# Performance work log

Hardware: AMD Instinct MI355X
Metric: run time of the kernel (lower is better)

The kernel has to match this reference:

```python
import jax, jax.numpy as jnp
import numpy as np

# Config: AydinConfig(hidden_dim=1024, intermediate_dim=2048, num_experts=8, top_k=2)
E, H, I, K = 8, 1024, 2048, 2
B, S = 4, 2048


def setup_inputs() -> dict:
    key = jax.random.key(0)
    k1, k2, k3, k4 = jax.random.split(key, 4)
    x = jax.random.normal(k1, (B, S, H), dtype=jnp.float32)
    # nn.Linear(H, E, bias=False): weight shape (E, H), default init ~ U(-1/sqrt(H), 1/sqrt(H))
    router_w = jax.random.uniform(k2, (E, H), dtype=jnp.float32,
                                  minval=-1.0, maxval=1.0) / np.sqrt(H).astype(np.float32)
    # normal init, std=0.02 (reset_parameters)
    w13 = jax.random.normal(k3, (E, H, 2 * I), dtype=jnp.float32) * 0.02
    w2 = jax.random.normal(k4, (E, I, H), dtype=jnp.float32) * 0.02
    return {"x": x, "router_w": router_w, "w13": w13, "w2": w2}


def reference(x, router_w, w13, w2):
    # Router: logits (B,S,E) -> softmax -> top-k with renormalized weights
    logits = jnp.einsum('bsh,eh->bse', x, router_w)
    probs = jax.nn.softmax(logits, axis=-1)
    weights, indices = jax.lax.top_k(probs, K)            # (B,S,K)
    weights = weights / (weights.sum(axis=-1, keepdims=True) + 1e-6)
    # Expert SwiGLU, computed densely over all experts then gathered.
    # Same math as the torch per-token weight gather, but avoids the
    # (B,S,K,H,2I) gathered-weight blowup.
    h13 = jnp.einsum('bsh,ehi->bsei', x, w13)             # (B,S,E,2I)
    gate, up = jnp.split(h13, 2, axis=-1)                 # (B,S,E,I) each
    h = jax.nn.silu(gate) * up
    y = jnp.einsum('bsei,eih->bseh', h, w2)               # (B,S,E,H)
    # Gather top-k expert outputs and combine with routing weights
    y_sel = jnp.take_along_axis(y, indices[..., None], axis=2)  # (B,S,K,H)
    return (y_sel * weights[..., None]).sum(axis=2)       # (B,S,H)
```

## Files before the change

kernel.cpp:

```cpp
#include <hip/hip_runtime.h>
#include <hip/hip_bf16.h>
#include <math.h>

#define NEXP 8
#define HD 1024
#define ID 2048
#define NTOK 8192
#define NROWS 16384

typedef __bf16 bf16_t;
typedef __bf16 bf16x8 __attribute__((ext_vector_type(8)));
typedef float f32x4 __attribute__((ext_vector_type(4)));

#define BK 64
#define MAXT1 72
#define MAXT2 136

__device__ __forceinline__ void gl16(const void* g, void* l) {
    __builtin_amdgcn_global_load_lds(
        (const __attribute__((address_space(1))) unsigned int*)g,
        (__attribute__((address_space(3))) unsigned int*)l, 16, 0, 0);
}

__global__ __launch_bounds__(256)
void router_kernel(const float* __restrict__ x, const float* __restrict__ rw,
                   bf16_t* __restrict__ xb, int* __restrict__ topk_idx,
                   float* __restrict__ topk_w)
{
    const int t = blockIdx.x;
    const int tid = threadIdx.x;
    const float4 xv = ((const float4*)(x + (size_t)t * HD))[tid];
    float acc[NEXP];
#pragma unroll
    for (int e = 0; e < NEXP; ++e) {
        const float4 w4 = ((const float4*)(rw + e * HD))[tid];
        acc[e] = xv.x * w4.x + xv.y * w4.y + xv.z * w4.z + xv.w * w4.w;
    }
    bf16_t tmp[4] = {(bf16_t)xv.x, (bf16_t)xv.y, (bf16_t)xv.z, (bf16_t)xv.w};
    *(uint2*)(xb + (size_t)t * HD + tid * 4) = *(const uint2*)tmp;

    __shared__ float red[4][NEXP];
    const int lane = tid & 63, wv = tid >> 6;
#pragma unroll
    for (int e = 0; e < NEXP; ++e) {
        float v = acc[e];
#pragma unroll
        for (int off = 32; off >= 1; off >>= 1) v += __shfl_down(v, off, 64);
        if (lane == 0) red[wv][e] = v;
    }
    __syncthreads();
    if (tid == 0) {
        float lg[NEXP], mx = -1e30f;
#pragma unroll
        for (int e = 0; e < NEXP; ++e) {
            lg[e] = red[0][e] + red[1][e] + red[2][e] + red[3][e];
            mx = fmaxf(mx, lg[e]);
        }
        float p[NEXP], s = 0.f;
#pragma unroll
        for (int e = 0; e < NEXP; ++e) { p[e] = __expf(lg[e] - mx); s += p[e]; }
        const float inv = 1.f / s;
#pragma unroll
        for (int e = 0; e < NEXP; ++e) p[e] *= inv;
        int i0 = 0; float p0 = p[0];
#pragma unroll
        for (int e = 1; e < NEXP; ++e) if (p[e] > p0) { p0 = p[e]; i0 = e; }
        int i1 = -1; float p1 = -1.f;
#pragma unroll
        for (int e = 0; e < NEXP; ++e) if (e != i0 && p[e] > p1) { p1 = p[e]; i1 = e; }
        const float d = 1.f / (p0 + p1 + 1e-6f);
        topk_idx[t * 2 + 0] = i0; topk_idx[t * 2 + 1] = i1;
        topk_w[t * 2 + 0] = p0 * d; topk_w[t * 2 + 1] = p1 * d;
    }
}

__global__ __launch_bounds__(256)
void count_kernel(const int* __restrict__ topk_idx, int* __restrict__ counts)
{
    __shared__ int lc[NEXP];
    const int tid = threadIdx.x;
    if (tid < NEXP) lc[tid] = 0;
    __syncthreads();
    const int t = blockIdx.x * 256 + tid;
    atomicAdd(&lc[topk_idx[t * 2 + 0]], 1);
    atomicAdd(&lc[topk_idx[t * 2 + 1]], 1);
    __syncthreads();
    if (tid < NEXP) atomicAdd(&counts[tid], lc[tid]);
}

__global__ void scan_kernel(const int* __restrict__ counts, int* __restrict__ offsets,
                            int* __restrict__ cursor,
                            unsigned* __restrict__ map256, unsigned* __restrict__ map128)
{
    __shared__ int tb2[NEXP + 1], tb1[NEXP + 1];
    if (threadIdx.x == 0) {
        int s = 0, t2 = 0, t1 = 0;
        for (int e = 0; e < NEXP; ++e) {
            offsets[e] = s; cursor[e] = s; s += counts[e];
            tb2[e] = t2; t2 += (counts[e] + 255) >> 8;
            tb1[e] = t1; t1 += (counts[e] + 127) >> 7;
        }
        tb2[NEXP] = t2; tb1[NEXP] = t1;
    }
    __syncthreads();
    for (int i = threadIdx.x; i < MAXT1; i += 64) {
        unsigned v = 0xFFFFFFFFu;
#pragma unroll
        for (int e = 0; e < NEXP; ++e)
            if (i >= tb2[e] && i < tb2[e + 1]) v = ((unsigned)e << 16) | (unsigned)(i - tb2[e]);
        map256[i] = v;
    }
    for (int i = threadIdx.x; i < MAXT2; i += 64) {
        unsigned v = 0xFFFFFFFFu;
#pragma unroll
        for (int e = 0; e < NEXP; ++e)
            if (i >= tb1[e] && i < tb1[e + 1]) v = ((unsigned)e << 16) | (unsigned)(i - tb1[e]);
        map128[i] = v;
    }
}

__global__ __launch_bounds__(256)
void scatter_kernel(const int* __restrict__ topk_idx, const float* __restrict__ topk_w,
                    int* __restrict__ cursor, int* __restrict__ token_list,
                    float* __restrict__ row_w, int* __restrict__ row_pos)
{
    __shared__ int lc[NEXP], gbase[NEXP];
    const int tid = threadIdx.x;
    if (tid < NEXP) lc[tid] = 0;
    __syncthreads();
    const int t = blockIdx.x * 256 + tid;
    const int e0 = topk_idx[t * 2 + 0], e1 = topk_idx[t * 2 + 1];
    const int lp0 = atomicAdd(&lc[e0], 1);
    const int lp1 = atomicAdd(&lc[e1], 1);
    __syncthreads();
    if (tid < NEXP) gbase[tid] = atomicAdd(&cursor[tid], lc[tid]);
    __syncthreads();
    const int p0 = gbase[e0] + lp0, p1 = gbase[e1] + lp1;
    token_list[p0] = t; row_w[p0] = topk_w[t * 2 + 0]; row_pos[t * 2 + 0] = p0;
    token_list[p1] = t; row_w[p1] = topk_w[t * 2 + 1]; row_pos[t * 2 + 1] = p1;
}

__global__ __launch_bounds__(256)
void precast_kernel(const float* __restrict__ src, bf16_t* __restrict__ dst,
                    int K, int N)
{
    const int e = blockIdx.z;
    src += (size_t)e * K * N;
    dst += (size_t)e * K * N;
    const int n0 = blockIdx.x * 64, k0 = blockIdx.y * 64;
    __shared__ float tile[64][65];
    const int tid = threadIdx.x;
    const int tx = (tid & 15) * 4, ty = tid >> 4;
#pragma unroll
    for (int p = 0; p < 4; ++p) {
        const float4 v = *(const float4*)(src + (size_t)(k0 + ty + p * 16) * N + n0 + tx);
        tile[ty + p * 16][tx + 0] = v.x;
        tile[ty + p * 16][tx + 1] = v.y;
        tile[ty + p * 16][tx + 2] = v.z;
        tile[ty + p * 16][tx + 3] = v.w;
    }
    __syncthreads();
    const int n = tid >> 2, kc = (tid & 3) * 16;
    bf16_t outv[16];
#pragma unroll
    for (int j = 0; j < 16; ++j) outv[j] = (bf16_t)tile[kc + j][n];
    bf16_t* d = dst + (size_t)(n0 + n) * K + k0 + kc;
    *(uint4*)d = *(uint4*)outv;
    *(uint4*)(d + 8) = *((uint4*)outv + 1);
}

__global__ __launch_bounds__(512)
void gemm1_kernel(const bf16_t* __restrict__ xb, const bf16_t* __restrict__ w13b,
                  const int* __restrict__ offsets, const int* __restrict__ counts,
                  const int* __restrict__ token_list,
                  const unsigned* __restrict__ tile_map, bf16_t* __restrict__ hbuf)
{
    const unsigned tm = tile_map[blockIdx.y];
    if (tm == 0xFFFFFFFFu) return;
    const int e = (int)(tm >> 16), mt = (int)(tm & 0xFFFFu);
    const int rows = counts[e];
    const int row_base = offsets[e];
    const int r0 = mt * 256;
    const int n0 = blockIdx.x * 64;

    __shared__ alignas(16) bf16_t As[256][64];
    __shared__ alignas(16) bf16_t Bg[64][64];
    __shared__ alignas(16) bf16_t Bu[64][64];

    const int tid = threadIdx.x;
    const int lane = tid & 63;
    const int wv = tid >> 6;
    const int wr = wv >> 1, wc = wv & 1;
    const int ln15 = lane & 15, q = lane >> 4;
    const int x7 = ln15 & 7;
    const int c0 = ((q ^ x7)) * 8;
    const int c1 = c0 ^ 32;

    const int srow = tid >> 3;
    const int scol = ((tid & 7) ^ ((tid >> 3) & 7)) * 8;
    const bf16_t* ap[4];
#pragma unroll
    for (int p = 0; p < 4; ++p) {
        int gr = row_base + r0 + p * 64 + srow;
        if (gr > NROWS - 1) gr = NROWS - 1;
        ap[p] = xb + (size_t)token_list[gr] * HD + scol;
    }
    const bf16_t* wb = w13b + (size_t)e * HD * (2 * ID);
    const bf16_t* bgp = wb + (size_t)(n0 + srow) * HD + scol;
    const bf16_t* bup = wb + (size_t)(ID + n0 + srow) * HD + scol;
    bf16_t* const d_bg = &Bg[0][0] + tid * 8;
    bf16_t* const d_bu = &Bu[0][0] + tid * 8;

    f32x4 accG[4][2], accU[4][2];
#pragma unroll
    for (int i = 0; i < 4; ++i)
#pragma unroll
        for (int j = 0; j < 2; ++j)
#pragma unroll
            for (int c = 0; c < 4; ++c) { accG[i][j][c] = 0.f; accU[i][j][c] = 0.f; }

    for (int k0 = 0; k0 < HD; k0 += BK) {
#pragma unroll
        for (int p = 0; p < 4; ++p) {
            gl16(ap[p], &As[0][0] + (p * 512 + tid) * 8);
            ap[p] += BK;
        }
        gl16(bgp, d_bg); gl16(bup, d_bu);
        bgp += BK; bup += BK;
        __syncthreads();

#pragma unroll
        for (int kk = 0; kk < 2; ++kk) {
            const int cc = kk ? c1 : c0;
            bf16x8 af[4], bgf[2], buf_[2];
#pragma unroll
            for (int i = 0; i < 4; ++i)
                af[i] = *(const bf16x8*)&As[wr * 64 + i * 16 + ln15][cc];
#pragma unroll
            for (int j = 0; j < 2; ++j) {
                bgf[j]  = *(const bf16x8*)&Bg[wc * 32 + j * 16 + ln15][cc];
                buf_[j] = *(const bf16x8*)&Bu[wc * 32 + j * 16 + ln15][cc];
            }
#pragma unroll
            for (int i = 0; i < 4; ++i)
#pragma unroll
                for (int j = 0; j < 2; ++j) {
                    accG[i][j] = __builtin_amdgcn_mfma_f32_16x16x32_bf16(af[i], bgf[j], accG[i][j], 0, 0, 0);
                    accU[i][j] = __builtin_amdgcn_mfma_f32_16x16x32_bf16(af[i], buf_[j], accU[i][j], 0, 0, 0);
                }
        }
        __syncthreads();
    }

#pragma unroll
    for (int i = 0; i < 4; ++i) {
#pragma unroll
        for (int reg = 0; reg < 4; ++reg) {
            const int rr = wr * 64 + i * 16 + q * 4 + reg;
            if (r0 + rr < rows) {
                bf16_t* dst = hbuf + (size_t)(row_base + r0 + rr) * ID + n0 + wc * 32 + ln15;
#pragma unroll
                for (int j = 0; j < 2; ++j) {
                    const float g = accG[i][j][reg], u = accU[i][j][reg];
                    dst[j * 16] = (bf16_t)((g / (1.f + __expf(-g))) * u);
                }
            }
        }
    }
}

__global__ __launch_bounds__(512)
void gemm2_kernel(const bf16_t* __restrict__ hbuf, const bf16_t* __restrict__ w2b,
                  const int* __restrict__ offsets, const int* __restrict__ counts,
                  const float* __restrict__ row_w,
                  const unsigned* __restrict__ tile_map, float* __restrict__ ybuf)
{
    const unsigned tm = tile_map[blockIdx.y];
    if (tm == 0xFFFFFFFFu) return;
    const int e = (int)(tm >> 16), mt = (int)(tm & 0xFFFFu);
    const int rows = counts[e];
    const int row_base = offsets[e];
    const int r0 = mt * 128;
    const int n0 = blockIdx.x * 128;

    __shared__ alignas(16) bf16_t As[128][64];
    __shared__ alignas(16) bf16_t Bs[128][64];
    __shared__ float rww_s[128];

    const int tid = threadIdx.x;
    if (tid < 128) {
        int gr = row_base + r0 + tid; if (gr > NROWS - 1) gr = NROWS - 1;
        rww_s[tid] = row_w[gr];
    }
    const int lane = tid & 63;
    const int wv = tid >> 6;
    const int wr = wv >> 1, wc = wv & 1;
    const int ln15 = lane & 15, q = lane >> 4;
    const int x7 = ln15 & 7;
    const int c0 = ((q ^ x7)) * 8;
    const int c1 = c0 ^ 32;

    const int srow = tid >> 3;
    const int scol = ((tid & 7) ^ ((tid >> 3) & 7)) * 8;
    const bf16_t* ap[2];
#pragma unroll
    for (int p = 0; p < 2; ++p) {
        int gr = row_base + r0 + p * 64 + srow;
        if (gr > NROWS - 1) gr = NROWS - 1;
        ap[p] = hbuf + (size_t)gr * ID + scol;
    }
    const bf16_t* w2e = w2b + (size_t)e * ID * HD;
    const bf16_t* bp0 = w2e + (size_t)(n0 + srow) * ID + scol;
    const bf16_t* bp1 = w2e + (size_t)(n0 + 64 + srow) * ID + scol;

    f32x4 acc[2][4];
#pragma unroll
    for (int i = 0; i < 2; ++i)
#pragma unroll
        for (int j = 0; j < 4; ++j)
#pragma unroll
            for (int c = 0; c < 4; ++c) acc[i][j][c] = 0.f;

    for (int k0 = 0; k0 < ID; k0 += BK) {
        gl16(ap[0], &As[0][0] + tid * 8);
        gl16(ap[1], &As[64][0] + tid * 8);
        gl16(bp0, &Bs[0][0] + tid * 8);
        gl16(bp1, &Bs[64][0] + tid * 8);
        ap[0] += BK; ap[1] += BK; bp0 += BK; bp1 += BK;
        __syncthreads();

#pragma unroll
        for (int kk = 0; kk < 2; ++kk) {
            const int cc = kk ? c1 : c0;
            bf16x8 af[2], bf_[4];
#pragma unroll
            for (int i = 0; i < 2; ++i)
                af[i] = *(const bf16x8*)&As[wr * 32 + i * 16 + ln15][cc];
#pragma unroll
            for (int j = 0; j < 4; ++j)
                bf_[j] = *(const bf16x8*)&Bs[wc * 64 + j * 16 + ln15][cc];
#pragma unroll
            for (int i = 0; i < 2; ++i)
#pragma unroll
                for (int j = 0; j < 4; ++j)
                    acc[i][j] = __builtin_amdgcn_mfma_f32_16x16x32_bf16(af[i], bf_[j], acc[i][j], 0, 0, 0);
        }
        __syncthreads();
    }

#pragma unroll
    for (int i = 0; i < 2; ++i) {
#pragma unroll
        for (int reg = 0; reg < 4; ++reg) {
            const int rr = wr * 32 + i * 16 + q * 4 + reg;
            if (r0 + rr < rows) {
                const float w = rww_s[rr];
                float* dst = ybuf + (size_t)(row_base + r0 + rr) * HD + n0 + wc * 64 + ln15;
#pragma unroll
                for (int j = 0; j < 4; ++j)
                    dst[j * 16] = acc[i][j][reg] * w;
            }
        }
    }
}

__global__ __launch_bounds__(256)
void combine_kernel(const float* __restrict__ ybuf, const int* __restrict__ row_pos,
                    float* __restrict__ out)
{
    const int t = blockIdx.x;
    const int p0 = row_pos[t * 2 + 0], p1 = row_pos[t * 2 + 1];
    const float4 a = ((const float4*)(ybuf + (size_t)p0 * HD))[threadIdx.x];
    const float4 b = ((const float4*)(ybuf + (size_t)p1 * HD))[threadIdx.x];
    float4 o; o.x = a.x + b.x; o.y = a.y + b.y; o.z = a.z + b.z; o.w = a.w + b.w;
    ((float4*)(out + (size_t)t * HD))[threadIdx.x] = o;
}

extern "C" void kernel_launch(void* const* d_in, const int* in_sizes, int n_in,
                              void* d_out, int out_size, void* d_ws, size_t ws_size,
                              hipStream_t stream) {
    const float* x   = (const float*)d_in[0];
    const float* rw  = (const float*)d_in[1];
    const float* w13 = (const float*)d_in[2];
    const float* w2  = (const float*)d_in[3];
    float* out = (float*)d_out;

    char* ws = (char*)d_ws;
    int*      counts     = (int*)(ws + 0);
    int*      cursor     = (int*)(ws + 64);
    int*      offsets    = (int*)(ws + 128);
    int*      topk_idx   = (int*)(ws + 256);
    float*    topk_w     = (float*)(ws + 256 + 1 * 65536);
    int*      token_list = (int*)(ws + 256 + 2 * 65536);
    float*    row_w      = (float*)(ws + 256 + 3 * 65536);
    int*      row_pos    = (int*)(ws + 256 + 4 * 65536);
    unsigned* map256     = (unsigned*)(ws + 256 + 5 * 65536);
    unsigned* map128     = (unsigned*)(ws + 256 + 6 * 65536);
    const size_t MB = 1024 * 1024;
    bf16_t* xb   = (bf16_t*)(ws + 1 * MB);
    bf16_t* hbuf = (bf16_t*)(ws + 17 * MB);
    bf16_t* w13b = (bf16_t*)(ws + 81 * MB);
    float*  ybuf = (float*)(ws + 81 * MB);
    bf16_t* w2b  = (bf16_t*)(ws + 145 * MB);

    hipMemsetAsync(ws, 0, 256, stream);

    dim3 gp1(2 * ID / 64, HD / 64, NEXP);
    precast_kernel<<<gp1, 256, 0, stream>>>(w13, w13b, HD, 2 * ID);
    dim3 gp2(HD / 64, ID / 64, NEXP);
    precast_kernel<<<gp2, 256, 0, stream>>>(w2, w2b, ID, HD);

    router_kernel<<<NTOK, 256, 0, stream>>>(x, rw, xb, topk_idx, topk_w);
    count_kernel<<<NTOK / 256, 256, 0, stream>>>(topk_idx, counts);
    scan_kernel<<<1, 64, 0, stream>>>(counts, offsets, cursor, map256, map128);
    scatter_kernel<<<NTOK / 256, 256, 0, stream>>>(topk_idx, topk_w, cursor,
                                                   token_list, row_w, row_pos);

    dim3 g1(ID / 64, MAXT1);
    gemm1_kernel<<<g1, 512, 0, stream>>>(xb, w13b, offsets, counts, token_list,
                                         map256, hbuf);
    dim3 g2(HD / 128, MAXT2);
    gemm2_kernel<<<g2, 512, 0, stream>>>(hbuf, w2b, offsets, counts, row_w,
                                         map128, ybuf);
    combine_kernel<<<NTOK, 256, 0, stream>>>(ybuf, row_pos, out);
}
```

Before: 580.9 us.

## Double gemm2 K-tile to 128 and remap gemm1 block order across tiles

gemm2 now stages 128-wide K slices of activations and w2 per iteration, using a 16-column XOR swizzle. This halves the number of barrier-separated loop iterations and doubles LDS usage to about 64KB per block. gemm1 linearizes and permutes its block IDs, interleaving groups of 8 so that neighbouring workgroups, likely landing on different XCDs, cover different tiles for cache locality. The remap hardcodes a grid shape of 32 by 72 (288 = 2304/8), which must match the launch configuration.

```diff
diff --git a/kernel.cpp b/kernel.cpp
--- a/kernel.cpp
+++ b/kernel.cpp
@@ -12,7 +12,8 @@
 typedef __bf16 bf16x8 __attribute__((ext_vector_type(8)));
 typedef float f32x4 __attribute__((ext_vector_type(4)));
 
-#define BK 64
+#define BK1 64
+#define BK2 128
 #define MAXT1 72
 #define MAXT2 136
 
@@ -175,13 +176,15 @@
                   const int* __restrict__ token_list,
                   const unsigned* __restrict__ tile_map, bf16_t* __restrict__ hbuf)
 {
-    const unsigned tm = tile_map[blockIdx.y];
+    unsigned id = blockIdx.y * 32u + blockIdx.x;
+    id = (id & 7u) * 288u + (id >> 3);
+    const unsigned tm = tile_map[id >> 5];
     if (tm == 0xFFFFFFFFu) return;
     const int e = (int)(tm >> 16), mt = (int)(tm & 0xFFFFu);
     const int rows = counts[e];
     const int row_base = offsets[e];
     const int r0 = mt * 256;
-    const int n0 = blockIdx.x * 64;
+    const int n0 = (int)(id & 31u) * 64;
 
     __shared__ alignas(16) bf16_t As[256][64];
     __shared__ alignas(16) bf16_t Bg[64][64];
@@ -219,14 +222,14 @@
 #pragma unroll
             for (int c = 0; c < 4; ++c) { accG[i][j][c] = 0.f; accU[i][j][c] = 0.f; }
 
-    for (int k0 = 0; k0 < HD; k0 += BK) {
+    for (int k0 = 0; k0 < HD; k0 += BK1) {
 #pragma unroll
         for (int p = 0; p < 4; ++p) {
             gl16(ap[p], &As[0][0] + (p * 512 + tid) * 8);
-            ap[p] += BK;
+            ap[p] += BK1;
         }
         gl16(bgp, d_bg); gl16(bup, d_bu);
-        bgp += BK; bup += BK;
+        bgp += BK1; bup += BK1;
         __syncthreads();
 
 #pragma unroll
@@ -283,8 +286,8 @@
     const int r0 = mt * 128;
     const int n0 = blockIdx.x * 128;
 
-    __shared__ alignas(16) bf16_t As[128][64];
-    __shared__ alignas(16) bf16_t Bs[128][64];
+    __shared__ alignas(16) bf16_t As[128][128];
+    __shared__ alignas(16) bf16_t Bs[128][128];
     __shared__ float rww_s[128];
 
     const int tid = threadIdx.x;
@@ -296,22 +299,19 @@
     const int wv = tid >> 6;
     const int wr = wv >> 1, wc = wv & 1;
     const int ln15 = lane & 15, q = lane >> 4;
-    const int x7 = ln15 & 7;
-    const int c0 = ((q ^ x7)) * 8;
-    const int c1 = c0 ^ 32;
-
-    const int srow = tid >> 3;
-    const int scol = ((tid & 7) ^ ((tid >> 3) & 7)) * 8;
-    const bf16_t* ap[2];
-#pragma unroll
-    for (int p = 0; p < 2; ++p) {
-        int gr = row_base + r0 + p * 64 + srow;
+
+    const int srow = tid >> 4;
+    const int scol = ((tid & 15) ^ ((tid >> 4) & 15)) * 8;
+    const bf16_t* ap[4];
+    const bf16_t* bp[4];
+    const bf16_t* w2e = w2b + (size_t)e * ID * HD;
+#pragma unroll
+    for (int p = 0; p < 4; ++p) {
+        int gr = row_base + r0 + p * 32 + srow;
         if (gr > NROWS - 1) gr = NROWS - 1;
         ap[p] = hbuf + (size_t)gr * ID + scol;
-    }
-    const bf16_t* w2e = w2b + (size_t)e * ID * HD;
-    const bf16_t* bp0 = w2e + (size_t)(n0 + srow) * ID + scol;
-    const bf16_t* bp1 = w2e + (size_t)(n0 + 64 + srow) * ID + scol;
+        bp[p] = w2e + (size_t)(n0 + p * 32 + srow) * ID + scol;
+    }
 
     f32x4 acc[2][4];
 #pragma unroll
@@ -321,17 +321,18 @@
 #pragma unroll
             for (int c = 0; c < 4; ++c) acc[i][j][c] = 0.f;
 
-    for (int k0 = 0; k0 < ID; k0 += BK) {
-        gl16(ap[0], &As[0][0] + tid * 8);
-        gl16(ap[1], &As[64][0] + tid * 8);
-        gl16(bp0, &Bs[0][0] + tid * 8);
-        gl16(bp1, &Bs[64][0] + tid * 8);
-        ap[0] += BK; ap[1] += BK; bp0 += BK; bp1 += BK;
+    for (int k0 = 0; k0 < ID; k0 += BK2) {
+#pragma unroll
+        for (int p = 0; p < 4; ++p) {
+            gl16(ap[p], &As[0][0] + (p * 512 + tid) * 8);
+            gl16(bp[p], &Bs[0][0] + (p * 512 + tid) * 8);
+            ap[p] += BK2; bp[p] += BK2;
+        }
         __syncthreads();
 
 #pragma unroll
-        for (int kk = 0; kk < 2; ++kk) {
-            const int cc = kk ? c1 : c0;
+        for (int kk = 0; kk < 4; ++kk) {
+            const int cc = ((kk * 4 + q) ^ ln15) * 8;
             bf16x8 af[2], bf_[4];
 #pragma unroll
             for (int i = 0; i < 2; ++i)
```

New measurement: 566.6 us. 2.5% less time.
